# Kernel optimization log

Hardware: AMD Instinct MI355X
Metric: run time of the kernel (lower is better)

The kernel has to match this reference:

```python
import jax, jax.numpy as jnp
import numpy as np

B, S, D, H, DFF = 8, 1024, 1024, 16, 4096
DK = D // H
NEG = -1000000000.0


def layernorm(x, g, b, eps=1e-5):
    mu = jnp.mean(x, axis=-1, keepdims=True)
    var = jnp.mean((x - mu) ** 2, axis=-1, keepdims=True)
    return (x - mu) / jnp.sqrt(var + eps) * g + b


def setup_inputs() -> dict:
    key = jax.random.key(0)
    ks = jax.random.split(key, 16)
    s = 0.02
    inp = {
        "x": jax.random.normal(ks[0], (B, S, D), jnp.float32),
        "binary_mask": jax.random.randint(ks[1], (B, S), 0, 2, jnp.int32),
        # per-head projections stacked: [H, D, DK]
        "Wq": jax.random.normal(ks[2], (H, D, DK), jnp.float32) * s,
        "bq": jnp.zeros((H, DK), jnp.float32),
        "Wk": jax.random.normal(ks[3], (H, D, DK), jnp.float32) * s,
        "bk": jnp.zeros((H, DK), jnp.float32),
        "Wv": jax.random.normal(ks[4], (H, D, DK), jnp.float32) * s,
        "bv": jnp.zeros((H, DK), jnp.float32),
        "Wo": jax.random.normal(ks[5], (D, D), jnp.float32) * s,
        "bo": jnp.zeros((D,), jnp.float32),
        "ga": jnp.ones((D,), jnp.float32),
        "ba": jnp.zeros((D,), jnp.float32),
        "W1": jax.random.normal(ks[6], (D, DFF), jnp.float32) * s,
        "b1": jnp.zeros((DFF,), jnp.float32),
        "W2": jax.random.normal(ks[7], (DFF, D), jnp.float32) * s,
        "b2": jnp.zeros((D,), jnp.float32),
        "gf": jnp.ones((D,), jnp.float32),
        "bf": jnp.zeros((D,), jnp.float32),
    }
    return inp


def encoder_fwd(x, binary_mask, Wq, bq, Wk, bk, Wv, bv, Wo, bo, ga, ba, W1, b1, W2, b2, gf, bf):
    # --- multi-head self-attention (heads vectorized over h axis) ---
    q = jnp.einsum("bsd,hdk->bhsk", x, Wq) + bq[None, :, None, :]
    k = jnp.einsum("bsd,hdk->bhsk", x, Wk) + bk[None, :, None, :]
    v = jnp.einsum("bsd,hdk->bhsk", x, Wv) + bv[None, :, None, :]
    score = jnp.einsum("bhik,bhjk->bhij", q, k) / jnp.sqrt(jnp.float32(DK))
    # mask: binary_mask is over KEY positions, broadcast over query dim
    score = score + jnp.where(binary_mask[:, None, None, :] == 0, NEG, 0.0)
    # NOTE: original code softmaxes over dim=1 of [B,Sq,Sk] -> the QUERY axis
    probs = jax.nn.softmax(score, axis=2)
    ctx = jnp.einsum("bhij,bhjk->bhik", probs, v)  # [B,H,S,DK]
    ctx = jnp.transpose(ctx, (0, 2, 1, 3)).reshape(x.shape[0], x.shape[1], D)
    attn_out = ctx @ Wo + bo
    y = layernorm(x + attn_out, ga, ba)
    # --- FFN ---
    h = jax.nn.relu(y @ W1 + b1)
    ffn_out = h @ W2 + b2
    return layernorm(y + ffn_out, gf, bf)


def reference(x, binary_mask, Wq, bq, Wk, bk, Wv, bv, Wo, bo, ga, ba, W1, b1, W2, b2, gf, bf):
    return encoder_fwd(x, binary_mask, Wq, bq, Wk, bk, Wv, bv, Wo, bo, ga, ba, W1, b1, W2, b2, gf, bf)
```

## Files before the change

kernel.cpp:

```cpp
#include <hip/hip_runtime.h>
#include <hip/hip_bf16.h>

typedef __bf16 bf16;
typedef __bf16 bf16x8 __attribute__((ext_vector_type(8)));
typedef __bf16 bf16x4 __attribute__((ext_vector_type(4)));
typedef float  f32x4  __attribute__((ext_vector_type(4)));

#define NB 8
#define NS 1024
#define ND 1024
#define NH 16
#define NDK 64
#define NDFF 4096

static __device__ __forceinline__ f32x4 mfma16(bf16x8 a, bf16x8 b, f32x4 c) {
    return __builtin_amdgcn_mfma_f32_16x16x32_bf16(a, b, c, 0, 0, 0);
}

#define GLDS(g, l) __builtin_amdgcn_global_load_lds( \
    (const __attribute__((address_space(1))) void*)(g), \
    (__attribute__((address_space(3))) void*)(l), 16, 0, 0)

__global__ __launch_bounds__(256) void prep_all(
    const float* __restrict__ x, const int* __restrict__ mask,
    const float* __restrict__ Wq, const float* __restrict__ Wk, const float* __restrict__ Wv,
    const float* __restrict__ Wo, const float* __restrict__ W1, const float* __restrict__ W2,
    const float* __restrict__ bq, const float* __restrict__ bk, const float* __restrict__ bv,
    bf16* __restrict__ xb, bf16* __restrict__ wqkvT, bf16* __restrict__ WoT,
    bf16* __restrict__ W1T, bf16* __restrict__ W2T, float* __restrict__ bqkv,
    int* __restrict__ newpos, int* __restrict__ Ucnt, float* __restrict__ cvec)
{
    __shared__ __align__(16) char shraw[64 * 65 * 4];
    int bid = blockIdx.x, t = threadIdx.x;
    if (bid < 8192) {
        int idx = bid * 256 + t;
        float4 v = ((const float4*)x)[idx];
        bf16x4 o = { (bf16)v.x, (bf16)v.y, (bf16)v.z, (bf16)v.w };
        ((bf16x4*)xb)[idx] = o;
    } else if (bid < 11264) {
        float (*T)[65] = (float (*)[65])shraw;
        int tb = bid - 8192;
        const float* src; bf16* dst; int srcLd, dstLd, tR, tC; bool scale = false;
        if (tb < 768) {
            int mat = tb >> 4, ty = tb & 15;
            int h = mat & 15, type = mat >> 4;
            const float* W = (type == 0) ? Wq : (type == 1 ? Wk : Wv);
            src = W + (size_t)h * ND * NDK;
            srcLd = NDK; tR = ty * 64; tC = 0;
            dst = wqkvT + ((size_t)type * 1024 + h * 64) * ND;
            dstLd = ND;
            scale = (type == 0);
        } else if (tb < 1024) {
            int b2 = tb - 768; int ty = b2 >> 4, tx = b2 & 15;
            src = Wo; srcLd = ND; tR = ty * 64; tC = tx * 64; dst = WoT; dstLd = ND;
        } else if (tb < 2048) {
            int b2 = tb - 1024; int ty = b2 >> 6, tx = b2 & 63;
            src = W1; srcLd = NDFF; tR = ty * 64; tC = tx * 64; dst = W1T; dstLd = ND;
        } else {
            int b2 = tb - 2048; int ty = b2 >> 4, tx = b2 & 15;
            src = W2; srcLd = ND; tR = ty * 64; tC = tx * 64; dst = W2T; dstLd = NDFF;
        }
        int c0 = t & 63, r0 = t >> 6;
        #pragma unroll
        for (int rr = 0; rr < 16; rr++) {
            int row = rr * 4 + r0;
            T[row][c0] = src[(size_t)(tR + row) * srcLd + tC + c0];
        }
        __syncthreads();
        #pragma unroll
        for (int cc = 0; cc < 16; cc++) {
            int col = cc * 4 + r0;
            float v = T[c0][col];
            if (scale) v *= 0.125f;
            dst[(size_t)(tC + col) * dstLd + tR + c0] = (bf16)v;
        }
    } else if (bid < 11276) {
        int n = (bid - 11264) * 256 + t;
        if (n < 3072) {
            int type = n >> 10, hk = n & 1023;
            const float* bb = (type == 0) ? bq : (type == 1 ? bk : bv);
            float v = bb[hk];
            if (type == 0) v *= 0.125f;
            bqkv[n] = v;
        }
    } else if (bid < 11284) {
        int* sums  = (int*)shraw;
        int* scans = (int*)(shraw + 1024);
        int b = bid - 11276;
        const int* mb = mask + b * NS;
        int m[4], s = 0;
        #pragma unroll
        for (int k = 0; k < 4; k++) { m[k] = (mb[t * 4 + k] != 0) ? 1 : 0; s += m[k]; }
        sums[t] = s;
        __syncthreads();
        if (t == 0) {
            int acc = 0;
            for (int i = 0; i < 256; i++) { scans[i] = acc; acc += sums[i]; }
            scans[256] = acc;
            Ucnt[b] = acc;
        }
        __syncthreads();
        int U = scans[256];
        int p = scans[t];
        #pragma unroll
        for (int k = 0; k < 4; k++) {
            int j = t * 4 + k;
            newpos[b * NS + j] = m[k] ? p : U + (j - p);
            p += m[k];
        }
    } else {
        float4 z = {0.f, 0.f, 0.f, 0.f};
        ((float4*)cvec)[(bid - 11284) * 256 + t] = z;
    }
}

__device__ __forceinline__ void gemm_bt_core(
    const bf16* __restrict__ A, const bf16* __restrict__ BT, int K,
    int rowBase, int colBase, f32x4 (&acc)[4][4], bf16* As, bf16* Bs)
{
    const int tid = threadIdx.x;
    const int lane = tid & 63, wid = tid >> 6;
    const int wr = (wid >> 1) * 64, wc = (wid & 1) * 64;
    const int lrow = lane & 15, lq = lane >> 4;
    const int srow = wid * 32 + (lane >> 3);
    const int gblk = (lane & 7) ^ ((lane >> 3) & 7);
    const bf16* Arow = A + (size_t)(rowBase + srow) * K + gblk * 8;
    const bf16* Brow = BT + (size_t)(colBase + srow) * K + gblk * 8;
    const int co0 = ((lq) ^ (lrow & 7)) * 8;
    const int co1 = ((4 + lq) ^ (lrow & 7)) * 8;
    f32x4 zz = {0.f, 0.f, 0.f, 0.f};
    #pragma unroll
    for (int i = 0; i < 4; i++)
        #pragma unroll
        for (int j = 0; j < 4; j++) acc[i][j] = zz;
    for (int k0 = 0; k0 < K; k0 += 64) {
        __syncthreads();
        #pragma unroll
        for (int it = 0; it < 4; it++)
            GLDS(Arow + (size_t)it * 8 * K + k0, As + (wid * 32 + it * 8) * 64);
        #pragma unroll
        for (int it = 0; it < 4; it++)
            GLDS(Brow + (size_t)it * 8 * K + k0, Bs + (wid * 32 + it * 8) * 64);
        __syncthreads();
        #pragma unroll
        for (int kh = 0; kh < 2; kh++) {
            const int co = kh ? co1 : co0;
            bf16x8 af[4], bfr[4];
            #pragma unroll
            for (int tt = 0; tt < 4; tt++) {
                af[tt]  = *(const bf16x8*)&As[(wr + tt * 16 + lrow) * 64 + co];
                bfr[tt] = *(const bf16x8*)&Bs[(wc + tt * 16 + lrow) * 64 + co];
            }
            #pragma unroll
            for (int i = 0; i < 4; i++)
                #pragma unroll
                for (int j = 0; j < 4; j++)
                    acc[i][j] = mfma16(af[i], bfr[j], acc[i][j]);
        }
    }
}

__device__ __forceinline__ void gemm8p(
    const bf16* __restrict__ A, const bf16* __restrict__ BT, int K,
    int rowBase, int colBase, f32x4 (&acc)[8][4], bf16* As, bf16* Bs)
{
    constexpr int SETSZ = 256 * 64;
    const int tid = threadIdx.x, lane = tid & 63, wid = tid >> 6;
    const int wm = wid >> 2, wn = wid & 3;
    const int lrow = lane & 15, lq = lane >> 4;
    const int s8 = lane >> 3, gblk = (lane & 7) ^ s8;
    const int co0 = (lq ^ (lrow & 7)) * 8;
    const int co1 = ((4 + lq) ^ (lrow & 7)) * 8;
    f32x4 zz = {0.f, 0.f, 0.f, 0.f};
    #pragma unroll
    for (int i = 0; i < 8; i++)
        #pragma unroll
        for (int j = 0; j < 4; j++) acc[i][j] = zz;
    const bf16* Ag = A  + (size_t)(rowBase + wid * 8 + s8) * K + gblk * 8;
    const bf16* Bg = BT + (size_t)(colBase + wid * 8 + s8) * K + gblk * 8;

#define SG_A(kt, set, h) do { \
    GLDS(Ag + (size_t)((h) * 128) * K + (kt) * 64, \
         As + (set) * SETSZ + ((h) * 128 + wid * 8) * 64); \
    GLDS(Ag + (size_t)((h) * 128 + 64) * K + (kt) * 64, \
         As + (set) * SETSZ + ((h) * 128 + 64 + wid * 8) * 64); \
} while (0)
#define SG_B(kt, set, h) do { \
    GLDS(Bg + (size_t)((h) * 128) * K + (kt) * 64, \
         Bs + (set) * SETSZ + ((h) * 128 + wid * 8) * 64); \
    GLDS(Bg + (size_t)((h) * 128 + 64) * K + (kt) * 64, \
         Bs + (set) * SETSZ + ((h) * 128 + 64 + wid * 8) * 64); \
} while (0)
#define RD_A(dst, base, ms) do { _Pragma("unroll") for (int i_ = 0; i_ < 4; i_++) { \
    int ro_ = (wm * 128 + (ms) * 64 + i_ * 16 + lrow) * 64; \
    dst[i_][0] = *(const bf16x8*)&(base)[ro_ + co0]; \
    dst[i_][1] = *(const bf16x8*)&(base)[ro_ + co1]; } } while (0)
#define RD_B(dst, base, ns) do { _Pragma("unroll") for (int j_ = 0; j_ < 2; j_++) { \
    int ro_ = (wn * 64 + (ns) * 32 + j_ * 16 + lrow) * 64; \
    dst[j_][0] = *(const bf16x8*)&(base)[ro_ + co0]; \
    dst[j_][1] = *(const bf16x8*)&(base)[ro_ + co1]; } } while (0)
#define CL8(av, bv, ms, ns) do { \
    __builtin_amdgcn_s_setprio(1); \
    _Pragma("unroll") for (int i_ = 0; i_ < 4; i_++) \
    _Pragma("unroll") for (int j_ = 0; j_ < 2; j_++) { \
        acc[(ms) * 4 + i_][(ns) * 2 + j_] = \
            mfma16(av[i_][0], bv[j_][0], acc[(ms) * 4 + i_][(ns) * 2 + j_]); \
        acc[(ms) * 4 + i_][(ns) * 2 + j_] = \
            mfma16(av[i_][1], bv[j_][1], acc[(ms) * 4 + i_][(ns) * 2 + j_]); } \
    __builtin_amdgcn_s_setprio(0); \
} while (0)
#define BAR8 __builtin_amdgcn_s_barrier()
#define VM4 asm volatile("s_waitcnt vmcnt(4)" ::: "memory")
#define VM0 asm volatile("s_waitcnt vmcnt(0)" ::: "memory")

    const int nt = K >> 6, nIter = nt >> 1;
    SG_B(0, 0, 0); SG_B(0, 0, 1);
    SG_A(0, 0, 0); SG_A(0, 0, 1);
    SG_B(1, 1, 0); SG_B(1, 1, 1);
    VM4; BAR8;
    const bf16* A0b = As;           const bf16* B0b = Bs;
    const bf16* A1b = As + SETSZ;   const bf16* B1b = Bs + SETSZ;
    for (int J = 0; J < nIter; ++J) {
        const int v = 2 * J + 1;
        const bool pf = (J + 1 < nIter);
        bf16x8 a0[4][2], a1[4][2], b0[2][2], b1[2][2];
        RD_A(a0, A0b, 0); RD_B(b0, B0b, 0);
        SG_A(v, 1, 0);
        BAR8; CL8(a0, b0, 0, 0); BAR8;
        RD_B(b1, B0b, 1);
        SG_A(v, 1, 1);
        BAR8; CL8(a0, b1, 0, 1); BAR8;
        RD_A(a1, A0b, 1);
        if (pf) SG_B(v + 1, 0, 0);
        BAR8; CL8(a1, b1, 1, 1); BAR8;
        if (pf) SG_B(v + 1, 0, 1);
        BAR8; CL8(a1, b0, 1, 0);
        if (pf) { VM4; } else { VM0; }
        BAR8;
        RD_A(a0, A1b, 0); RD_B(b0, B1b, 0);
        if (pf) SG_A(v + 1, 0, 0);
        BAR8; CL8(a0, b0, 0, 0); BAR8;
        RD_B(b1, B1b, 1);
        if (pf) SG_A(v + 1, 0, 1);
        BAR8; CL8(a0, b1, 0, 1); BAR8;
        RD_A(a1, A1b, 1);
        if (pf) SG_B(v + 2, 1, 0);
        BAR8; CL8(a1, b1, 1, 1); BAR8;
        if (pf) SG_B(v + 2, 1, 1);
        BAR8; CL8(a1, b0, 1, 0);
        if (pf) { VM4; } else { VM0; }
        BAR8;
    }
#undef SG_A
#undef SG_B
#undef RD_A
#undef RD_B
#undef CL8
#undef BAR8
#undef VM4
#undef VM0
}

__device__ __forceinline__ void gemmB_core(
    const bf16* __restrict__ A, const bf16* __restrict__ BT, int K,
    int rowBase, int colBase, f32x4 (&acc)[4][4], bf16* As, bf16* Bs)
{
    constexpr int ABUF = 128 * 64, BBUF = 256 * 64;
    const int tid = threadIdx.x, lane = tid & 63, wid = tid >> 6;
    const int wm = wid >> 2, wn = wid & 3;
    const int lrow = lane & 15, lq = lane >> 4;
    const int srow = lane >> 3, gblk = (lane & 7) ^ srow;
    const int co0 = (lq ^ (lrow & 7)) * 8;
    const int co1 = ((4 + lq) ^ (lrow & 7)) * 8;
    f32x4 zz = {0.f, 0.f, 0.f, 0.f};
    #pragma unroll
    for (int i = 0; i < 4; i++)
        #pragma unroll
        for (int j = 0; j < 4; j++) acc[i][j] = zz;
    const bf16* Ag = A  + (size_t)(rowBase + wid * 8 + srow) * K + gblk * 8;
    const bf16* Bg = BT + (size_t)(colBase + wid * 8 + srow) * K + gblk * 8;

#define SGA2(kt, bi, rr) GLDS(Ag + (size_t)(kt) * 64 + (size_t)(rr) * 64 * K, \
                              As + (bi) * ABUF + ((rr) * 64 + wid * 8) * 64)
#define SGB2(kt, bi, rr) GLDS(Bg + (size_t)(kt) * 64 + (size_t)(rr) * 64 * K, \
                              Bs + (bi) * BBUF + ((rr) * 64 + wid * 8) * 64)
#define RDA2() do { _Pragma("unroll") for (int i_ = 0; i_ < 4; i_++) { \
    int ro_ = (wm * 64 + i_ * 16 + lrow) * 64; \
    af[i_][0] = *(const bf16x8*)&Ab[ro_ + co0]; \
    af[i_][1] = *(const bf16x8*)&Ab[ro_ + co1]; } } while (0)
#define RDB2(dst, NS_) do { _Pragma("unroll") for (int j_ = 0; j_ < 2; j_++) { \
    int ro_ = (wn * 64 + (NS_) * 32 + j_ * 16 + lrow) * 64; \
    dst[j_][0] = *(const bf16x8*)&Bb[ro_ + co0]; \
    dst[j_][1] = *(const bf16x8*)&Bb[ro_ + co1]; } } while (0)
#define CLUSTER_B(bfx, JO) do { \
    __builtin_amdgcn_s_barrier(); \
    asm volatile("s_waitcnt lgkmcnt(0)" ::: "memory"); \
    __builtin_amdgcn_sched_barrier(0); \
    __builtin_amdgcn_s_setprio(1); \
    _Pragma("unroll") \
    for (int i_ = 0; i_ < 4; i_++) \
        _Pragma("unroll") \
        for (int j_ = 0; j_ < 2; j_++) { \
            acc[i_][(JO) + j_] = mfma16(af[i_][0], bfx[j_][0], acc[i_][(JO) + j_]); \
            acc[i_][(JO) + j_] = mfma16(af[i_][1], bfx[j_][1], acc[i_][(JO) + j_]); \
        } \
    __builtin_amdgcn_s_setprio(0); \
} while (0)

    const int nt = K >> 6;
    SGA2(0, 0, 0); SGA2(0, 0, 1);
    SGB2(0, 0, 0); SGB2(0, 0, 1); SGB2(0, 0, 2); SGB2(0, 0, 3);
    SGA2(1, 1, 0); SGA2(1, 1, 1);
    SGB2(1, 1, 0); SGB2(1, 1, 1); SGB2(1, 1, 2); SGB2(1, 1, 3);
    asm volatile("s_waitcnt vmcnt(6)" ::: "memory");
    __builtin_amdgcn_s_barrier();

    int ci = 0, si = 2;
    for (int t = 0; t < nt; ++t) {
        const bf16* Ab = As + ci * ABUF;
        const bf16* Bb = Bs + ci * BBUF;
        const bool pf = (t + 2 < nt);
        bf16x8 af[4][2], bf0[2][2], bf1[2][2];
        RDA2(); RDB2(bf0, 0);
        if (pf) { SGA2(t + 2, si, 0); SGA2(t + 2, si, 1); SGB2(t + 2, si, 0); SGB2(t + 2, si, 1); }
        CLUSTER_B(bf0, 0);
        __builtin_amdgcn_s_barrier();
        RDB2(bf1, 1);
        if (pf) { SGB2(t + 2, si, 2); SGB2(t + 2, si, 3); }
        CLUSTER_B(bf1, 2);
        if (pf)                asm volatile("s_waitcnt vmcnt(6)" ::: "memory");
        else if (t + 1 < nt)   asm volatile("s_waitcnt vmcnt(0)" ::: "memory");
        __builtin_amdgcn_s_barrier();
        ci = (ci == 2) ? 0 : ci + 1;
        si = (si == 2) ? 0 : si + 1;
    }
#undef SGA2
#undef SGB2
#undef RDA2
#undef RDB2
#undef CLUSTER_B
}

__global__ __launch_bounds__(512, 2) void g1_qkv(
    const bf16* __restrict__ x, const bf16* __restrict__ wqkvT, const float* __restrict__ bqkv,
    const int* __restrict__ newpos,
    bf16* __restrict__ Q, bf16* __restrict__ Kb, bf16* __restrict__ Vb)
{
    __shared__ bf16 As[3 * 128 * 64], Bs[3 * 256 * 64];
    f32x4 acc[4][4];
    int g = blockIdx.x;
    int sw = (g & 7) * 96 + (g >> 3);
    int bm = sw / 12, bn = sw % 12;
    int rowBase = bm * 128, colBase = bn * 256;
    gemmB_core(x, wqkvT, ND, rowBase, colBase, acc, As, Bs);
    const int tid = threadIdx.x, lane = tid & 63, wid = tid >> 6;
    const int wm = wid >> 2, wn = wid & 3, lrow = lane & 15, lq = lane >> 4;
    const int type = colBase >> 10;
    int spv[4][4];
    if (type != 0) {
        #pragma unroll
        for (int i = 0; i < 4; i++)
            #pragma unroll
            for (int r = 0; r < 4; r++) {
                int grow = rowBase + wm * 64 + i * 16 + lq * 4 + r;
                spv[i][r] = newpos[grow];
            }
    }
    #pragma unroll
    for (int j = 0; j < 4; j++) {
        int gcol = colBase + wn * 64 + j * 16 + lrow;
        float bias = bqkv[gcol];
        int h = (gcol >> 6) & 15, kk = gcol & 63;
        bf16* dst = (type == 0) ? Q : (type == 1 ? Kb : Vb);
        #pragma unroll
        for (int i = 0; i < 4; i++) {
            #pragma unroll
            for (int r = 0; r < 4; r++) {
                int grow = rowBase + wm * 64 + i * 16 + lq * 4 + r;
                int b = grow >> 10;
                int s = (type == 0) ? (grow & 1023) : spv[i][r];
                dst[((size_t)(b * NH + h) * NS + s) * NDK + kk] = (bf16)(acc[i][j][r] + bias);
            }
        }
    }
}

__global__ __launch_bounds__(256) void vt_trans(
    const bf16* __restrict__ Vb, const int* __restrict__ Ucnt,
    bf16* __restrict__ Vt, float* __restrict__ cvec)
{
    __shared__ bf16 T[64 * 72];
    __shared__ float red[4][64];
    int bh = blockIdx.y, s0 = blockIdx.x * 64;
    const bf16* src = Vb + ((size_t)bh * NS + s0) * NDK;
    int tid = threadIdx.x;
    #pragma unroll
    for (int it = 0; it < 2; it++) {
        int g = tid + it * 256;
        int row = g >> 3, c = (g & 7) * 8;
        *(bf16x8*)&T[row * 72 + c] = *(const bf16x8*)&src[row * NDK + c];
    }
    __syncthreads();
    #pragma unroll
    for (int it = 0; it < 2; it++) {
        int g = tid + it * 256;
        int kk = g >> 3, sc = (g & 7) * 8;
        bf16x8 v;
        #pragma unroll
        for (int t = 0; t < 8; t++) v[t] = T[(sc + t) * 72 + kk];
        *(bf16x8*)&Vt[((size_t)bh * NDK + kk) * NS + s0 + sc] = v;
    }
    int U = Ucnt[bh >> 4];
    int lo = U - s0;
    if (lo < 0) lo = 0;
    if (lo < 64) {
        int kk = tid & 63, ss = tid >> 6;
        float a = 0.f;
        for (int r = lo + ss; r < 64; r += 4) a += (float)T[r * 72 + kk];
        red[ss][kk] = a;
        __syncthreads();
        if (ss == 0)
            atomicAdd(&cvec[bh * 64 + kk], red[0][kk] + red[1][kk] + red[2][kk] + red[3][kk]);
    }
}

__global__ __launch_bounds__(256) void g2_stats(
    const bf16* __restrict__ Q, const bf16* __restrict__ Kb,
    const int* __restrict__ Ucnt, float2* __restrict__ alpha)
{
    __shared__ bf16 Qs[128 * 64];
    int bh = blockIdx.y, b = bh >> 4;
    int jBase = blockIdx.x * 128;
    int U = Ucnt[b];
    const int tid = threadIdx.x;
    if (jBase >= U) {
        if (tid < 128) {
            float2 z; z.x = 0.f; z.y = 0.f;
            alpha[(size_t)bh * NS + jBase + tid] = z;
        }
        return;
    }
    const bf16* Kp = Kb + (size_t)bh * NS * NDK;
    const bf16* Qp = Q + (size_t)bh * NS * NDK;
    const int lane = tid & 63, wid = tid >> 6;
    const int lrow = lane & 15, lq = lane >> 4;
    bf16x8 kf[2][2];
    #pragma unroll
    for (int jt = 0; jt < 2; jt++)
        #pragma unroll
        for (int kh = 0; kh < 2; kh++)
            kf[jt][kh] = *(const bf16x8*)&Kp[(size_t)(jBase + wid * 32 + jt * 16 + lrow) * NDK + kh * 32 + lq * 8];
    const int srow = lane >> 3;
    const int gblk = (lane & 7) ^ srow;
    float Lacc[2][4];
    #pragma unroll
    for (int jt = 0; jt < 2; jt++)
        #pragma unroll
        for (int r = 0; r < 4; r++) Lacc[jt][r] = 0.f;
    f32x4 zz = {0.f, 0.f, 0.f, 0.f};
    for (int i0 = 0; i0 < NS; i0 += 128) {
        __syncthreads();
        #pragma unroll
        for (int it = 0; it < 4; it++)
            GLDS(Qp + (size_t)(i0 + wid * 32 + it * 8 + srow) * NDK + gblk * 8,
                 Qs + (wid * 32 + it * 8) * 64);
        __syncthreads();
        #pragma unroll
        for (int it = 0; it < 8; it++) {
            bf16x8 qb[2];
            #pragma unroll
            for (int kh = 0; kh < 2; kh++)
                qb[kh] = *(const bf16x8*)&Qs[(it * 16 + lrow) * 64 + ((kh * 4 + lq) ^ (lrow & 7)) * 8];
            #pragma unroll
            for (int jt = 0; jt < 2; jt++) {
                f32x4 s = mfma16(kf[jt][0], qb[0], zz);
                s = mfma16(kf[jt][1], qb[1], s);
                #pragma unroll
                for (int r = 0; r < 4; r++) Lacc[jt][r] += __expf(s[r]);
            }
        }
    }
    #pragma unroll
    for (int jt = 0; jt < 2; jt++) {
        #pragma unroll
        for (int r = 0; r < 4; r++) {
            float v = Lacc[jt][r];
            v += __shfl_xor(v, 1); v += __shfl_xor(v, 2);
            v += __shfl_xor(v, 4); v += __shfl_xor(v, 8);
            if (lrow == 0) {
                int j = jBase + wid * 32 + jt * 16 + lq * 4 + r;
                float2 ac;
                ac.x = (j < U) ? 1.f / v : 0.f;
                ac.y = 0.f;
                alpha[(size_t)bh * NS + j] = ac;
            }
        }
    }
}

__global__ __launch_bounds__(256) void g3_ctx(
    const bf16* __restrict__ Q, const bf16* __restrict__ Kb, const bf16* __restrict__ Vt,
    const float2* __restrict__ alpha, const int* __restrict__ Ucnt,
    const float* __restrict__ cvec, bf16* __restrict__ ctx)
{
    __shared__ bf16 Ks[64 * 64];
    __shared__ bf16 Vs[64 * 64];
    __shared__ bf16 Ps[4 * 64 * 64];
    int bh = blockIdx.y, iBase = blockIdx.x * 256;
    int b = bh >> 4, h = bh & 15;
    int U = Ucnt[b];
    int Ur = (U + 63) & ~63;
    const bf16* Qp = Q + (size_t)bh * NS * NDK;
    const bf16* Kp = Kb + (size_t)bh * NS * NDK;
    const bf16* Vp = Vt + (size_t)bh * NDK * NS;
    const float2* al = alpha + (size_t)bh * NS;
    const int tid = threadIdx.x, lane = tid & 63, wid = tid >> 6;
    const int lrow = lane & 15, lq = lane >> 4;
    const int iw = iBase + wid * 64;
    bf16x8 qf[4][2];
    #pragma unroll
    for (int it = 0; it < 4; it++)
        #pragma unroll
        for (int kh = 0; kh < 2; kh++)
            qf[it][kh] = *(const bf16x8*)&Qp[(size_t)(iw + it * 16 + lrow) * NDK + kh * 32 + lq * 8];
    const int srow = lane >> 3;
    const int gblk = (lane & 7) ^ srow;
    f32x4 cacc[4][4];
    f32x4 zz = {0.f, 0.f, 0.f, 0.f};
    #pragma unroll
    for (int it = 0; it < 4; it++)
        #pragma unroll
        for (int kt = 0; kt < 4; kt++) cacc[it][kt] = zz;
    bf16* Pw = Ps + wid * 64 * 64;
    for (int j0 = 0; j0 < Ur; j0 += 64) {
        __syncthreads();
        #pragma unroll
        for (int it = 0; it < 2; it++)
            GLDS(Kp + (size_t)(j0 + wid * 16 + it * 8 + srow) * NDK + gblk * 8,
                 Ks + (wid * 16 + it * 8) * 64);
        #pragma unroll
        for (int it = 0; it < 2; it++)
            GLDS(Vp + (size_t)(wid * 16 + it * 8 + srow) * NS + j0 + gblk * 8,
                 Vs + (wid * 16 + it * 8) * 64);
        __syncthreads();
        bf16x8 kb[4][2];
        #pragma unroll
        for (int jt = 0; jt < 4; jt++)
            #pragma unroll
            for (int kh = 0; kh < 2; kh++)
                kb[jt][kh] = *(const bf16x8*)&Ks[(jt * 16 + lrow) * 64 + ((kh * 4 + lq) ^ (lrow & 7)) * 8];
        #pragma unroll
        for (int jt = 0; jt < 4; jt++) {
            float2 acj[4];
            #pragma unroll
            for (int r = 0; r < 4; r++) acj[r] = al[j0 + jt * 16 + lq * 4 + r];
            #pragma unroll
            for (int it = 0; it < 4; it++) {
                f32x4 s = mfma16(kb[jt][0], qf[it][0], zz);
                s = mfma16(kb[jt][1], qf[it][1], s);
                bf16x4 pv;
                #pragma unroll
                for (int r = 0; r < 4; r++)
                    pv[r] = (bf16)(acj[r].x * __expf(s[r]) + acj[r].y);
                int i = it * 16 + lrow;
                int jb = jt * 2 + (lq >> 1);
                *(bf16x4*)&Pw[i * 64 + ((jb ^ (i & 7)) * 8) + (lq & 1) * 4] = pv;
            }
        }
        bf16x8 vb[4][2];
        #pragma unroll
        for (int kt = 0; kt < 4; kt++)
            #pragma unroll
            for (int kh = 0; kh < 2; kh++)
                vb[kt][kh] = *(const bf16x8*)&Vs[(kt * 16 + lrow) * 64 + ((kh * 4 + lq) ^ (lrow & 7)) * 8];
        #pragma unroll
        for (int it = 0; it < 4; it++) {
            bf16x8 pa[2];
            #pragma unroll
            for (int kh = 0; kh < 2; kh++)
                pa[kh] = *(const bf16x8*)&Pw[(it * 16 + lrow) * 64 + ((kh * 4 + lq) ^ (lrow & 7)) * 8];
            #pragma unroll
            for (int kt = 0; kt < 4; kt++) {
                cacc[it][kt] = mfma16(pa[0], vb[kt][0], cacc[it][kt]);
                cacc[it][kt] = mfma16(pa[1], vb[kt][1], cacc[it][kt]);
            }
        }
    }
    #pragma unroll
    for (int kt = 0; kt < 4; kt++) {
        int col = h * NDK + kt * 16 + lrow;
        float cv = cvec[bh * 64 + kt * 16 + lrow] * (1.f / 1024.f);
        #pragma unroll
        for (int it = 0; it < 4; it++) {
            #pragma unroll
            for (int r = 0; r < 4; r++) {
                int i = iw + it * 16 + lq * 4 + r;
                ctx[(size_t)(b * NS + i) * ND + col] = (bf16)(cacc[it][kt][r] + cv);
            }
        }
    }
}

__global__ __launch_bounds__(256) void g4_proj(
    const bf16* __restrict__ ctx, const bf16* __restrict__ WoT, const float* __restrict__ bo,
    const bf16* __restrict__ xb, bf16* __restrict__ t1b)
{
    __shared__ bf16 As[128 * 64], Bs[128 * 64];
    f32x4 acc[4][4];
    int rowBase = blockIdx.x * 128, colBase = blockIdx.y * 128;
    gemm_bt_core(ctx, WoT, ND, rowBase, colBase, acc, As, Bs);
    const int tid = threadIdx.x, lane = tid & 63, wid = tid >> 6;
    const int wr = (wid >> 1) * 64, wc = (wid & 1) * 64, lrow = lane & 15, lq = lane >> 4;
    #pragma unroll
    for (int j = 0; j < 4; j++) {
        int gcol = colBase + wc + j * 16 + lrow;
        float bias = bo[gcol];
        #pragma unroll
        for (int i = 0; i < 4; i++) {
            #pragma unroll
            for (int r = 0; r < 4; r++) {
                int grow = rowBase + wr + i * 16 + lq * 4 + r;
                float v = acc[i][j][r] + bias + (float)xb[(size_t)grow * ND + gcol];
                t1b[(size_t)grow * ND + gcol] = (bf16)v;
            }
        }
    }
}

__global__ __launch_bounds__(512, 2) void g5_ffn1(
    const bf16* __restrict__ y, const bf16* __restrict__ W1T, const float* __restrict__ b1,
    bf16* __restrict__ hb)
{
    __shared__ bf16 As[2 * 256 * 64], Bs[2 * 256 * 64];
    f32x4 acc[8][4];
    int g = blockIdx.x;
    int sw = (g & 7) * 64 + (g >> 3);
    int bm = sw >> 4, bn = sw & 15;
    int rowBase = bm * 256, colBase = bn * 256;
    gemm8p(y, W1T, ND, rowBase, colBase, acc, As, Bs);
    const int tid = threadIdx.x, lane = tid & 63, wid = tid >> 6;
    const int wm = wid >> 2, wn = wid & 3, lrow = lane & 15, lq = lane >> 4;
    #pragma unroll
    for (int j = 0; j < 4; j++) {
        int gcol = colBase + wn * 64 + j * 16 + lrow;
        float bias = b1[gcol];
        #pragma unroll
        for (int i = 0; i < 8; i++) {
            #pragma unroll
            for (int r = 0; r < 4; r++) {
                int grow = rowBase + wm * 128 + i * 16 + lq * 4 + r;
                float v = fmaxf(acc[i][j][r] + bias, 0.f);
                hb[(size_t)grow * NDFF + gcol] = (bf16)v;
            }
        }
    }
}

__global__ __launch_bounds__(512, 2) void g6_ffn2(
    const bf16* __restrict__ hb, const bf16* __restrict__ W2T, const float* __restrict__ b2,
    const bf16* __restrict__ yb, bf16* __restrict__ zb)
{
    __shared__ bf16 As[3 * 128 * 64], Bs[3 * 256 * 64];
    f32x4 acc[4][4];
    int g = blockIdx.x;
    int sw = (g & 7) * 32 + (g >> 3);
    int bm = sw >> 2, bn = sw & 3;
    int rowBase = bm * 128, colBase = bn * 256;
    gemmB_core(hb, W2T, NDFF, rowBase, colBase, acc, As, Bs);
    const int tid = threadIdx.x, lane = tid & 63, wid = tid >> 6;
    const int wm = wid >> 2, wn = wid & 3, lrow = lane & 15, lq = lane >> 4;
    #pragma unroll
    for (int j = 0; j < 4; j++) {
        int gcol = colBase + wn * 64 + j * 16 + lrow;
        float bias = b2[gcol];
        #pragma unroll
        for (int i = 0; i < 4; i++) {
            #pragma unroll
            for (int r = 0; r < 4; r++) {
                int grow = rowBase + wm * 64 + i * 16 + lq * 4 + r;
                float v = acc[i][j][r] + bias + (float)yb[(size_t)grow * ND + gcol];
                zb[(size_t)grow * ND + gcol] = (bf16)v;
            }
        }
    }
}

__global__ __launch_bounds__(256) void ln_kernel(
    const bf16* __restrict__ in, bf16* __restrict__ outb, float* __restrict__ outf,
    const float* __restrict__ g, const float* __restrict__ bb)
{
    int row = blockIdx.x, tid = threadIdx.x;
    const bf16* p = in + (size_t)row * ND;
    bf16x4 v4 = *(const bf16x4*)&p[tid * 4];
    float vv[4] = {(float)v4[0], (float)v4[1], (float)v4[2], (float)v4[3]};
    float s = vv[0] + vv[1] + vv[2] + vv[3];
    float q = vv[0]*vv[0] + vv[1]*vv[1] + vv[2]*vv[2] + vv[3]*vv[3];
    #pragma unroll
    for (int m = 1; m < 64; m <<= 1) { s += __shfl_xor(s, m); q += __shfl_xor(q, m); }
    __shared__ float rs[4], rq[4];
    int wid = tid >> 6, lane = tid & 63;
    if (lane == 0) { rs[wid] = s; rq[wid] = q; }
    __syncthreads();
    s = rs[0] + rs[1] + rs[2] + rs[3];
    q = rq[0] + rq[1] + rq[2] + rq[3];
    float mean = s * (1.f / 1024.f);
    float var = q * (1.f / 1024.f) - mean * mean;
    float rstd = 1.f / sqrtf(var + 1e-5f);
    float4 of;
    bf16x4 ob;
    #pragma unroll
    for (int k = 0; k < 4; k++) {
        int col = tid * 4 + k;
        float yv = (vv[k] - mean) * rstd * g[col] + bb[col];
        ((float*)&of)[k] = yv;
        ob[k] = (bf16)yv;
    }
    if (outb) *(bf16x4*)&outb[(size_t)row * ND + tid * 4] = ob;
    if (outf) ((float4*)(outf + (size_t)row * ND))[tid] = of;
}

extern "C" void kernel_launch(void* const* d_in, const int* in_sizes, int n_in,
                              void* d_out, int out_size, void* d_ws, size_t ws_size,
                              hipStream_t stream)
{
    const float* x    = (const float*)d_in[0];
    const int*   mask = (const int*)d_in[1];
    const float* Wq   = (const float*)d_in[2];
    const float* bq   = (const float*)d_in[3];
    const float* Wk   = (const float*)d_in[4];
    const float* bk   = (const float*)d_in[5];
    const float* Wv   = (const float*)d_in[6];
    const float* bv   = (const float*)d_in[7];
    const float* Wo   = (const float*)d_in[8];
    const float* bo   = (const float*)d_in[9];
    const float* ga   = (const float*)d_in[10];
    const float* ba   = (const float*)d_in[11];
    const float* W1   = (const float*)d_in[12];
    const float* b1   = (const float*)d_in[13];
    const float* W2   = (const float*)d_in[14];
    const float* b2   = (const float*)d_in[15];
    const float* gf   = (const float*)d_in[16];
    const float* bfb  = (const float*)d_in[17];

    size_t off = 0;
    auto alloc = [&](size_t n) { char* p = (char*)d_ws + off; off += (n + 255) & ~(size_t)255; return (void*)p; };
    bf16*   wqkvT = (bf16*)  alloc((size_t)3072 * 1024 * 2);
    bf16*   WoT   = (bf16*)  alloc((size_t)1024 * 1024 * 2);
    bf16*   W1T   = (bf16*)  alloc((size_t)4096 * 1024 * 2);
    bf16*   W2T   = (bf16*)  alloc((size_t)1024 * 4096 * 2);
    float*  bqkv  = (float*) alloc(3072 * 4);
    float2* alpha = (float2*)alloc((size_t)NB * NH * NS * 8);
    int*    newpos= (int*)   alloc((size_t)NB * NS * 4);
    int*    Ucnt  = (int*)   alloc(NB * 4);
    float*  cvec  = (float*) alloc((size_t)NB * NH * NDK * 4);
    bf16*   xb    = (bf16*)  alloc((size_t)8192 * 1024 * 2);
    bf16*   ub    = (bf16*)  alloc((size_t)8192 * 4096 * 2);
    bf16*   Qb    = ub;
    bf16*   Kb    = ub + (size_t)8192 * 1024;
    bf16*   Vt    = ub + (size_t)2 * 8192 * 1024;
    bf16*   ctx   = ub + (size_t)3 * 8192 * 1024;
    bf16*   hb    = ub;
    bf16*   t1b   = (bf16*)  alloc((size_t)8192 * 1024 * 2);
    bf16*   Vb    = t1b;
    bf16*   zb    = t1b;
    bf16*   yb    = (bf16*)  alloc((size_t)8192 * 1024 * 2);

    prep_all<<<11292, 256, 0, stream>>>(x, mask, Wq, Wk, Wv, Wo, W1, W2, bq, bk, bv,
                                        xb, wqkvT, WoT, W1T, W2T, bqkv, newpos, Ucnt, cvec);
    g1_qkv<<<768, 512, 0, stream>>>(xb, wqkvT, bqkv, newpos, Qb, Kb, Vb);
    vt_trans<<<dim3(16, 128), 256, 0, stream>>>(Vb, Ucnt, Vt, cvec);
    g2_stats<<<dim3(8, 128), 256, 0, stream>>>(Qb, Kb, Ucnt, alpha);
    g3_ctx<<<dim3(4, 128), 256, 0, stream>>>(Qb, Kb, Vt, alpha, Ucnt, cvec, ctx);
    g4_proj<<<dim3(64, 8), 256, 0, stream>>>(ctx, WoT, bo, xb, t1b);
    ln_kernel<<<8192, 256, 0, stream>>>(t1b, yb, nullptr, ga, ba);
    g5_ffn1<<<512, 512, 0, stream>>>(yb, W1T, b1, hb);
    g6_ffn2<<<256, 512, 0, stream>>>(hb, W2T, b2, yb, zb);
    ln_kernel<<<8192, 256, 0, stream>>>(zb, nullptr, (float*)d_out, gf, bfb);
}
```

Before: 472.8 us.

## Fuse layernorms into GEMM kernels via grid barrier and merge V-transpose with stats

```diff
diff --git a/kernel.cpp b/kernel.cpp
--- a/kernel.cpp
+++ b/kernel.cpp
@@ -28,7 +28,8 @@
     const float* __restrict__ bq, const float* __restrict__ bk, const float* __restrict__ bv,
     bf16* __restrict__ xb, bf16* __restrict__ wqkvT, bf16* __restrict__ WoT,
     bf16* __restrict__ W1T, bf16* __restrict__ W2T, float* __restrict__ bqkv,
-    int* __restrict__ newpos, int* __restrict__ Ucnt, float* __restrict__ cvec)
+    int* __restrict__ newpos, int* __restrict__ Ucnt, float* __restrict__ cvec,
+    int* __restrict__ ctrs)
 {
     __shared__ __align__(16) char shraw[64 * 65 * 4];
     int bid = blockIdx.x, t = threadIdx.x;
@@ -111,53 +112,88 @@
     } else {
         float4 z = {0.f, 0.f, 0.f, 0.f};
         ((float4*)cvec)[(bid - 11284) * 256 + t] = z;
-    }
-}
-
-__device__ __forceinline__ void gemm_bt_core(
+        if (bid == 11284 && t < 2) ctrs[t] = 0;
+    }
+}
+
+__device__ __forceinline__ void gemmB_core(
     const bf16* __restrict__ A, const bf16* __restrict__ BT, int K,
     int rowBase, int colBase, f32x4 (&acc)[4][4], bf16* As, bf16* Bs)
 {
-    const int tid = threadIdx.x;
-    const int lane = tid & 63, wid = tid >> 6;
-    const int wr = (wid >> 1) * 64, wc = (wid & 1) * 64;
+    constexpr int ABUF = 128 * 64, BBUF = 256 * 64;
+    const int tid = threadIdx.x, lane = tid & 63, wid = tid >> 6;
+    const int wm = wid >> 2, wn = wid & 3;
     const int lrow = lane & 15, lq = lane >> 4;
-    const int srow = wid * 32 + (lane >> 3);
-    const int gblk = (lane & 7) ^ ((lane >> 3) & 7);
-    const bf16* Arow = A + (size_t)(rowBase + srow) * K + gblk * 8;
-    const bf16* Brow = BT + (size_t)(colBase + srow) * K + gblk * 8;
-    const int co0 = ((lq) ^ (lrow & 7)) * 8;
+    const int srow = lane >> 3, gblk = (lane & 7) ^ srow;
+    const int co0 = (lq ^ (lrow & 7)) * 8;
     const int co1 = ((4 + lq) ^ (lrow & 7)) * 8;
     f32x4 zz = {0.f, 0.f, 0.f, 0.f};
     #pragma unroll
     for (int i = 0; i < 4; i++)
         #pragma unroll
         for (int j = 0; j < 4; j++) acc[i][j] = zz;
-    for (int k0 = 0; k0 < K; k0 += 64) {
-        __syncthreads();
-        #pragma unroll
-        for (int it = 0; it < 4; it++)
-            GLDS(Arow + (size_t)it * 8 * K + k0, As + (wid * 32 + it * 8) * 64);
-        #pragma unroll
-        for (int it = 0; it < 4; it++)
-            GLDS(Brow + (size_t)it * 8 * K + k0, Bs + (wid * 32 + it * 8) * 64);
-        __syncthreads();
-        #pragma unroll
-        for (int kh = 0; kh < 2; kh++) {
-            const int co = kh ? co1 : co0;
-            bf16x8 af[4], bfr[4];
-            #pragma unroll
-            for (int tt = 0; tt < 4; tt++) {
-                af[tt]  = *(const bf16x8*)&As[(wr + tt * 16 + lrow) * 64 + co];
-                bfr[tt] = *(const bf16x8*)&Bs[(wc + tt * 16 + lrow) * 64 + co];
-            }
-            #pragma unroll
-            for (int i = 0; i < 4; i++)
-                #pragma unroll
-                for (int j = 0; j < 4; j++)
-                    acc[i][j] = mfma16(af[i], bfr[j], acc[i][j]);
-        }
-    }
+    const bf16* Ag = A  + (size_t)(rowBase + wid * 8 + srow) * K + gblk * 8;
+    const bf16* Bg = BT + (size_t)(colBase + wid * 8 + srow) * K + gblk * 8;
+
+#define SGA2(kt, bi, rr) GLDS(Ag + (size_t)(kt) * 64 + (size_t)(rr) * 64 * K, \
+                              As + (bi) * ABUF + ((rr) * 64 + wid * 8) * 64)
+#define SGB2(kt, bi, rr) GLDS(Bg + (size_t)(kt) * 64 + (size_t)(rr) * 64 * K, \
+                              Bs + (bi) * BBUF + ((rr) * 64 + wid * 8) * 64)
+#define RDA2() do { _Pragma("unroll") for (int i_ = 0; i_ < 4; i_++) { \
+    int ro_ = (wm * 64 + i_ * 16 + lrow) * 64; \
+    af[i_][0] = *(const bf16x8*)&Ab[ro_ + co0]; \
+    af[i_][1] = *(const bf16x8*)&Ab[ro_ + co1]; } } while (0)
+#define RDB2(dst, NS_) do { _Pragma("unroll") for (int j_ = 0; j_ < 2; j_++) { \
+    int ro_ = (wn * 64 + (NS_) * 32 + j_ * 16 + lrow) * 64; \
+    dst[j_][0] = *(const bf16x8*)&Bb[ro_ + co0]; \
+    dst[j_][1] = *(const bf16x8*)&Bb[ro_ + co1]; } } while (0)
+#define CLUSTER_B(bfx, JO) do { \
+    __builtin_amdgcn_s_barrier(); \
+    asm volatile("s_waitcnt lgkmcnt(0)" ::: "memory"); \
+    __builtin_amdgcn_sched_barrier(0); \
+    __builtin_amdgcn_s_setprio(1); \
+    _Pragma("unroll") \
+    for (int i_ = 0; i_ < 4; i_++) \
+        _Pragma("unroll") \
+        for (int j_ = 0; j_ < 2; j_++) { \
+            acc[i_][(JO) + j_] = mfma16(af[i_][0], bfx[j_][0], acc[i_][(JO) + j_]); \
+            acc[i_][(JO) + j_] = mfma16(af[i_][1], bfx[j_][1], acc[i_][(JO) + j_]); \
+        } \
+    __builtin_amdgcn_s_setprio(0); \
+} while (0)
+
+    const int nt = K >> 6;
+    SGA2(0, 0, 0); SGA2(0, 0, 1);
+    SGB2(0, 0, 0); SGB2(0, 0, 1); SGB2(0, 0, 2); SGB2(0, 0, 3);
+    SGA2(1, 1, 0); SGA2(1, 1, 1);
+    SGB2(1, 1, 0); SGB2(1, 1, 1); SGB2(1, 1, 2); SGB2(1, 1, 3);
+    asm volatile("s_waitcnt vmcnt(6)" ::: "memory");
+    __builtin_amdgcn_s_barrier();
+
+    int ci = 0, si = 2;
+    for (int t = 0; t < nt; ++t) {
+        const bf16* Ab = As + ci * ABUF;
+        const bf16* Bb = Bs + ci * BBUF;
+        const bool pf = (t + 2 < nt);
+        bf16x8 af[4][2], bf0[2][2], bf1[2][2];
+        RDA2(); RDB2(bf0, 0);
+        if (pf) { SGA2(t + 2, si, 0); SGA2(t + 2, si, 1); SGB2(t + 2, si, 0); SGB2(t + 2, si, 1); }
+        CLUSTER_B(bf0, 0);
+        __builtin_amdgcn_s_barrier();
+        RDB2(bf1, 1);
+        if (pf) { SGB2(t + 2, si, 2); SGB2(t + 2, si, 3); }
+        CLUSTER_B(bf1, 2);
+        if (pf)                asm volatile("s_waitcnt vmcnt(6)" ::: "memory");
+        else if (t + 1 < nt)   asm volatile("s_waitcnt vmcnt(0)" ::: "memory");
+        __builtin_amdgcn_s_barrier();
+        ci = (ci == 2) ? 0 : ci + 1;
+        si = (si == 2) ? 0 : si + 1;
+    }
+#undef SGA2
+#undef SGB2
+#undef RDA2
+#undef RDB2
+#undef CLUSTER_B
 }
 
 __device__ __forceinline__ void gemm8p(
@@ -261,84 +297,61 @@
 #undef VM0
 }
 
-__device__ __forceinline__ void gemmB_core(
-    const bf16* __restrict__ A, const bf16* __restrict__ BT, int K,
-    int rowBase, int colBase, f32x4 (&acc)[4][4], bf16* As, bf16* Bs)
-{
-    constexpr int ABUF = 128 * 64, BBUF = 256 * 64;
-    const int tid = threadIdx.x, lane = tid & 63, wid = tid >> 6;
-    const int wm = wid >> 2, wn = wid & 3;
-    const int lrow = lane & 15, lq = lane >> 4;
-    const int srow = lane >> 3, gblk = (lane & 7) ^ srow;
-    const int co0 = (lq ^ (lrow & 7)) * 8;
-    const int co1 = ((4 + lq) ^ (lrow & 7)) * 8;
-    f32x4 zz = {0.f, 0.f, 0.f, 0.f};
-    #pragma unroll
-    for (int i = 0; i < 4; i++)
-        #pragma unroll
-        for (int j = 0; j < 4; j++) acc[i][j] = zz;
-    const bf16* Ag = A  + (size_t)(rowBase + wid * 8 + srow) * K + gblk * 8;
-    const bf16* Bg = BT + (size_t)(colBase + wid * 8 + srow) * K + gblk * 8;
-
-#define SGA2(kt, bi, rr) GLDS(Ag + (size_t)(kt) * 64 + (size_t)(rr) * 64 * K, \
-                              As + (bi) * ABUF + ((rr) * 64 + wid * 8) * 64)
-#define SGB2(kt, bi, rr) GLDS(Bg + (size_t)(kt) * 64 + (size_t)(rr) * 64 * K, \
-                              Bs + (bi) * BBUF + ((rr) * 64 + wid * 8) * 64)
-#define RDA2() do { _Pragma("unroll") for (int i_ = 0; i_ < 4; i_++) { \
-    int ro_ = (wm * 64 + i_ * 16 + lrow) * 64; \
-    af[i_][0] = *(const bf16x8*)&Ab[ro_ + co0]; \
-    af[i_][1] = *(const bf16x8*)&Ab[ro_ + co1]; } } while (0)
-#define RDB2(dst, NS_) do { _Pragma("unroll") for (int j_ = 0; j_ < 2; j_++) { \
-    int ro_ = (wn * 64 + (NS_) * 32 + j_ * 16 + lrow) * 64; \
-    dst[j_][0] = *(const bf16x8*)&Bb[ro_ + co0]; \
-    dst[j_][1] = *(const bf16x8*)&Bb[ro_ + co1]; } } while (0)
-#define CLUSTER_B(bfx, JO) do { \
-    __builtin_amdgcn_s_barrier(); \
-    asm volatile("s_waitcnt lgkmcnt(0)" ::: "memory"); \
-    __builtin_amdgcn_sched_barrier(0); \
-    __builtin_amdgcn_s_setprio(1); \
-    _Pragma("unroll") \
-    for (int i_ = 0; i_ < 4; i_++) \
-        _Pragma("unroll") \
-        for (int j_ = 0; j_ < 2; j_++) { \
-            acc[i_][(JO) + j_] = mfma16(af[i_][0], bfx[j_][0], acc[i_][(JO) + j_]); \
-            acc[i_][(JO) + j_] = mfma16(af[i_][1], bfx[j_][1], acc[i_][(JO) + j_]); \
-        } \
-    __builtin_amdgcn_s_setprio(0); \
-} while (0)
-
-    const int nt = K >> 6;
-    SGA2(0, 0, 0); SGA2(0, 0, 1);
-    SGB2(0, 0, 0); SGB2(0, 0, 1); SGB2(0, 0, 2); SGB2(0, 0, 3);
-    SGA2(1, 1, 0); SGA2(1, 1, 1);
-    SGB2(1, 1, 0); SGB2(1, 1, 1); SGB2(1, 1, 2); SGB2(1, 1, 3);
-    asm volatile("s_waitcnt vmcnt(6)" ::: "memory");
-    __builtin_amdgcn_s_barrier();
-
-    int ci = 0, si = 2;
-    for (int t = 0; t < nt; ++t) {
-        const bf16* Ab = As + ci * ABUF;
-        const bf16* Bb = Bs + ci * BBUF;
-        const bool pf = (t + 2 < nt);
-        bf16x8 af[4][2], bf0[2][2], bf1[2][2];
-        RDA2(); RDB2(bf0, 0);
-        if (pf) { SGA2(t + 2, si, 0); SGA2(t + 2, si, 1); SGB2(t + 2, si, 0); SGB2(t + 2, si, 1); }
-        CLUSTER_B(bf0, 0);
-        __builtin_amdgcn_s_barrier();
-        RDB2(bf1, 1);
-        if (pf) { SGB2(t + 2, si, 2); SGB2(t + 2, si, 3); }
-        CLUSTER_B(bf1, 2);
-        if (pf)                asm volatile("s_waitcnt vmcnt(6)" ::: "memory");
-        else if (t + 1 < nt)   asm volatile("s_waitcnt vmcnt(0)" ::: "memory");
-        __builtin_amdgcn_s_barrier();
-        ci = (ci == 2) ? 0 : ci + 1;
-        si = (si == 2) ? 0 : si + 1;
-    }
-#undef SGA2
-#undef SGB2
-#undef RDA2
-#undef RDB2
-#undef CLUSTER_B
+__device__ __forceinline__ void grid_rendezvous(int* ctr, int nblocks)
+{
+    __threadfence();
+    __syncthreads();
+    if (threadIdx.x == 0) {
+        atomicAdd(ctr, 1);
+        while (atomicAdd(ctr, 0) < nblocks) __builtin_amdgcn_s_sleep(8);
+    }
+    __syncthreads();
+    __threadfence();
+}
+
+template<bool WRITE_F32>
+__device__ __forceinline__ void ln_rows(
+    const bf16* __restrict__ in, bf16* __restrict__ outb, float* __restrict__ outf,
+    const float* gv, const float* bv, int rowBase)
+{
+    const int lane = threadIdx.x & 63, wid = threadIdx.x >> 6;
+    #pragma unroll
+    for (int it = 0; it < 4; it++) {
+        int row = rowBase + it * 8 + wid;
+        const bf16* p = in + (size_t)row * ND + lane * 16;
+        bf16x8 v0 = *(const bf16x8*)p;
+        bf16x8 v1 = *(const bf16x8*)(p + 8);
+        float vv[16];
+        float s = 0.f, q = 0.f;
+        #pragma unroll
+        for (int k = 0; k < 8; k++) { vv[k] = (float)v0[k]; vv[8 + k] = (float)v1[k]; }
+        #pragma unroll
+        for (int k = 0; k < 16; k++) { s += vv[k]; q += vv[k] * vv[k]; }
+        #pragma unroll
+        for (int m = 1; m < 64; m <<= 1) { s += __shfl_xor(s, m); q += __shfl_xor(q, m); }
+        float mean = s * (1.f / 1024.f);
+        float var = q * (1.f / 1024.f) - mean * mean;
+        float rstd = 1.f / sqrtf(var + 1e-5f);
+        if (WRITE_F32) {
+            float4 o[4];
+            #pragma unroll
+            for (int k = 0; k < 16; k++)
+                ((float*)o)[k] = (vv[k] - mean) * rstd * gv[k] + bv[k];
+            float* dst = outf + (size_t)row * ND + lane * 16;
+            #pragma unroll
+            for (int k = 0; k < 4; k++) ((float4*)dst)[k] = o[k];
+        } else {
+            bf16x8 o0, o1;
+            #pragma unroll
+            for (int k = 0; k < 8; k++) {
+                o0[k] = (bf16)((vv[k] - mean) * rstd * gv[k] + bv[k]);
+                o1[k] = (bf16)((vv[8 + k] - mean) * rstd * gv[8 + k] + bv[8 + k]);
+            }
+            bf16* dst = outb + (size_t)row * ND + lane * 16;
+            *(bf16x8*)dst = o0;
+            *(bf16x8*)(dst + 8) = o1;
+        }
+    }
 }
 
 __global__ __launch_bounds__(512, 2) void g1_qkv(
@@ -385,54 +398,52 @@
     }
 }
 
-__global__ __launch_bounds__(256) void vt_trans(
-    const bf16* __restrict__ Vb, const int* __restrict__ Ucnt,
+__global__ __launch_bounds__(256) void g2v(
+    const bf16* __restrict__ Q, const bf16* __restrict__ Kb, const bf16* __restrict__ Vb,
+    const int* __restrict__ Ucnt, float2* __restrict__ alpha,
     bf16* __restrict__ Vt, float* __restrict__ cvec)
 {
-    __shared__ bf16 T[64 * 72];
-    __shared__ float red[4][64];
-    int bh = blockIdx.y, s0 = blockIdx.x * 64;
-    const bf16* src = Vb + ((size_t)bh * NS + s0) * NDK;
-    int tid = threadIdx.x;
-    #pragma unroll
-    for (int it = 0; it < 2; it++) {
-        int g = tid + it * 256;
-        int row = g >> 3, c = (g & 7) * 8;
-        *(bf16x8*)&T[row * 72 + c] = *(const bf16x8*)&src[row * NDK + c];
-    }
-    __syncthreads();
-    #pragma unroll
-    for (int it = 0; it < 2; it++) {
-        int g = tid + it * 256;
-        int kk = g >> 3, sc = (g & 7) * 8;
-        bf16x8 v;
-        #pragma unroll
-        for (int t = 0; t < 8; t++) v[t] = T[(sc + t) * 72 + kk];
-        *(bf16x8*)&Vt[((size_t)bh * NDK + kk) * NS + s0 + sc] = v;
-    }
-    int U = Ucnt[bh >> 4];
-    int lo = U - s0;
-    if (lo < 0) lo = 0;
-    if (lo < 64) {
-        int kk = tid & 63, ss = tid >> 6;
-        float a = 0.f;
-        for (int r = lo + ss; r < 64; r += 4) a += (float)T[r * 72 + kk];
-        red[ss][kk] = a;
+    __shared__ __align__(16) char sraw[128 * 64 * 2];
+    int bh = blockIdx.y, b = bh >> 4;
+    const int tid = threadIdx.x;
+    if (blockIdx.x >= 8) {
+        bf16* T = (bf16*)sraw;
+        float (*red)[64] = (float (*)[64])(sraw + 64 * 72 * 2);
+        int s0 = (blockIdx.x - 8) * 64;
+        const bf16* src = Vb + ((size_t)bh * NS + s0) * NDK;
+        #pragma unroll
+        for (int it = 0; it < 2; it++) {
+            int g = tid + it * 256;
+            int row = g >> 3, c = (g & 7) * 8;
+            *(bf16x8*)&T[row * 72 + c] = *(const bf16x8*)&src[row * NDK + c];
+        }
         __syncthreads();
-        if (ss == 0)
-            atomicAdd(&cvec[bh * 64 + kk], red[0][kk] + red[1][kk] + red[2][kk] + red[3][kk]);
-    }
-}
-
-__global__ __launch_bounds__(256) void g2_stats(
-    const bf16* __restrict__ Q, const bf16* __restrict__ Kb,
-    const int* __restrict__ Ucnt, float2* __restrict__ alpha)
-{
-    __shared__ bf16 Qs[128 * 64];
-    int bh = blockIdx.y, b = bh >> 4;
+        #pragma unroll
+        for (int it = 0; it < 2; it++) {
+            int g = tid + it * 256;
+            int kk = g >> 3, sc = (g & 7) * 8;
+            bf16x8 v;
+            #pragma unroll
+            for (int t = 0; t < 8; t++) v[t] = T[(sc + t) * 72 + kk];
+            *(bf16x8*)&Vt[((size_t)bh * NDK + kk) * NS + s0 + sc] = v;
+        }
+        int U = Ucnt[b];
+        int lo = U - s0;
+        if (lo < 0) lo = 0;
+        if (lo < 64) {
+            int kk = tid & 63, ss = tid >> 6;
+            float a = 0.f;
+            for (int r = lo + ss; r < 64; r += 4) a += (float)T[r * 72 + kk];
+            red[ss][kk] = a;
+            __syncthreads();
+            if (ss == 0)
+                atomicAdd(&cvec[bh * 64 + kk], red[0][kk] + red[1][kk] + red[2][kk] + red[3][kk]);
+        }
+        return;
+    }
+    bf16* Qs = (bf16*)sraw;
     int jBase = blockIdx.x * 128;
     int U = Ucnt[b];
-    const int tid = threadIdx.x;
     if (jBase >= U) {
         if (tid < 128) {
             float2 z; z.x = 0.f; z.y = 0.f;
@@ -601,30 +612,43 @@
     }
 }
 
-__global__ __launch_bounds__(256) void g4_proj(
+__global__ __launch_bounds__(512, 2) void g4_proj(
     const bf16* __restrict__ ctx, const bf16* __restrict__ WoT, const float* __restrict__ bo,
-    const bf16* __restrict__ xb, bf16* __restrict__ t1b)
-{
-    __shared__ bf16 As[128 * 64], Bs[128 * 64];
+    const bf16* __restrict__ xb, bf16* __restrict__ t1b,
+    const float* __restrict__ ga, const float* __restrict__ ba,
+    bf16* __restrict__ yb, int* __restrict__ ctr)
+{
+    __shared__ bf16 As[3 * 128 * 64], Bs[3 * 256 * 64];
     f32x4 acc[4][4];
-    int rowBase = blockIdx.x * 128, colBase = blockIdx.y * 128;
-    gemm_bt_core(ctx, WoT, ND, rowBase, colBase, acc, As, Bs);
+    int g = blockIdx.x;
+    int sw = (g & 7) * 32 + (g >> 3);
+    int bm = sw >> 2, bn = sw & 3;
+    int rowBase = bm * 128, colBase = bn * 256;
+    gemmB_core(ctx, WoT, ND, rowBase, colBase, acc, As, Bs);
     const int tid = threadIdx.x, lane = tid & 63, wid = tid >> 6;
-    const int wr = (wid >> 1) * 64, wc = (wid & 1) * 64, lrow = lane & 15, lq = lane >> 4;
+    const int wm = wid >> 2, wn = wid & 3, lrow = lane & 15, lq = lane >> 4;
     #pragma unroll
     for (int j = 0; j < 4; j++) {
-        int gcol = colBase + wc + j * 16 + lrow;
+        int gcol = colBase + wn * 64 + j * 16 + lrow;
         float bias = bo[gcol];
         #pragma unroll
         for (int i = 0; i < 4; i++) {
             #pragma unroll
             for (int r = 0; r < 4; r++) {
-                int grow = rowBase + wr + i * 16 + lq * 4 + r;
+                int grow = rowBase + wm * 64 + i * 16 + lq * 4 + r;
                 float v = acc[i][j][r] + bias + (float)xb[(size_t)grow * ND + gcol];
                 t1b[(size_t)grow * ND + gcol] = (bf16)v;
             }
         }
     }
+    float gv[16], bv[16];
+    #pragma unroll
+    for (int k = 0; k < 16; k++) {
+        int col = lane * 16 + k;
+        gv[k] = ga[col]; bv[k] = ba[col];
+    }
+    grid_rendezvous(ctr, 256);
+    ln_rows<false>(t1b, yb, nullptr, gv, bv, blockIdx.x * 32);
 }
 
 __global__ __launch_bounds__(512, 2) void g5_ffn1(
@@ -658,7 +682,9 @@
 
 __global__ __launch_bounds__(512, 2) void g6_ffn2(
     const bf16* __restrict__ hb, const bf16* __restrict__ W2T, const float* __restrict__ b2,
-    const bf16* __restrict__ yb, bf16* __restrict__ zb)
+    const bf16* __restrict__ yb, bf16* __restrict__ zb,
+    const float* __restrict__ gf, const float* __restrict__ bfb,
+    float* __restrict__ outf, int* __restrict__ ctr)
 {
     __shared__ bf16 As[3 * 128 * 64], Bs[3 * 256 * 64];
     f32x4 acc[4][4];
@@ -683,40 +709,14 @@
             }
         }
     }
-}
-
-__global__ __launch_bounds__(256) void ln_kernel(
-    const bf16* __restrict__ in, bf16* __restrict__ outb, float* __restrict__ outf,
-    const float* __restrict__ g, const float* __restrict__ bb)
-{
-    int row = blockIdx.x, tid = threadIdx.x;
-    const bf16* p = in + (size_t)row * ND;
-    bf16x4 v4 = *(const bf16x4*)&p[tid * 4];
-    float vv[4] = {(float)v4[0], (float)v4[1], (float)v4[2], (float)v4[3]};
-    float s = vv[0] + vv[1] + vv[2] + vv[3];
-    float q = vv[0]*vv[0] + vv[1]*vv[1] + vv[2]*vv[2] + vv[3]*vv[3];
-    #pragma unroll
-    for (int m = 1; m < 64; m <<= 1) { s += __shfl_xor(s, m); q += __shfl_xor(q, m); }
-    __shared__ float rs[4], rq[4];
-    int wid = tid >> 6, lane = tid & 63;
-    if (lane == 0) { rs[wid] = s; rq[wid] = q; }
-    __syncthreads();
-    s = rs[0] + rs[1] + rs[2] + rs[3];
-    q = rq[0] + rq[1] + rq[2] + rq[3];
-    float mean = s * (1.f / 1024.f);
-    float var = q * (1.f / 1024.f) - mean * mean;
-    float rstd = 1.f / sqrtf(var + 1e-5f);
-    float4 of;
-    bf16x4 ob;
-    #pragma unroll
-    for (int k = 0; k < 4; k++) {
-        int col = tid * 4 + k;
-        float yv = (vv[k] - mean) * rstd * g[col] + bb[col];
-        ((float*)&of)[k] = yv;
-        ob[k] = (bf16)yv;
-    }
-    if (outb) *(bf16x4*)&outb[(size_t)row * ND + tid * 4] = ob;
-    if (outf) ((float4*)(outf + (size_t)row * ND))[tid] = of;
+    float gv[16], bv[16];
+    #pragma unroll
+    for (int k = 0; k < 16; k++) {
+        int col = lane * 16 + k;
+        gv[k] = gf[col]; bv[k] = bfb[col];
+    }
+    grid_rendezvous(ctr, 256);
+    ln_rows<true>(zb, nullptr, outf, gv, bv, blockIdx.x * 32);
 }
 
 extern "C" void kernel_launch(void* const* d_in, const int* in_sizes, int n_in,
@@ -753,6 +753,7 @@
     int*    newpos= (int*)   alloc((size_t)NB * NS * 4);
     int*    Ucnt  = (int*)   alloc(NB * 4);
     float*  cvec  = (float*) alloc((size_t)NB * NH * NDK * 4);
+    int*    ctrs  = (int*)   alloc(8);
     bf16*   xb    = (bf16*)  alloc((size_t)8192 * 1024 * 2);
     bf16*   ub    = (bf16*)  alloc((size_t)8192 * 4096 * 2);
     bf16*   Qb    = ub;
@@ -766,14 +767,11 @@
     bf16*   yb    = (bf16*)  alloc((size_t)8192 * 1024 * 2);
 
     prep_all<<<11292, 256, 0, stream>>>(x, mask, Wq, Wk, Wv, Wo, W1, W2, bq, bk, bv,
-                                        xb, wqkvT, WoT, W1T, W2T, bqkv, newpos, Ucnt, cvec);
+                                        xb, wqkvT, WoT, W1T, W2T, bqkv, newpos, Ucnt, cvec, ctrs);
     g1_qkv<<<768, 512, 0, stream>>>(xb, wqkvT, bqkv, newpos, Qb, Kb, Vb);
-    vt_trans<<<dim3(16, 128), 256, 0, stream>>>(Vb, Ucnt, Vt, cvec);
-    g2_stats<<<dim3(8, 128), 256, 0, stream>>>(Qb, Kb, Ucnt, alpha);
+    g2v<<<dim3(24, 128), 256, 0, stream>>>(Qb, Kb, Vb, Ucnt, alpha, Vt, cvec);
     g3_ctx<<<dim3(4, 128), 256, 0, stream>>>(Qb, Kb, Vt, alpha, Ucnt, cvec, ctx);
-    g4_proj<<<dim3(64, 8), 256, 0, stream>>>(ctx, WoT, bo, xb, t1b);
-    ln_kernel<<<8192, 256, 0, stream>>>(t1b, yb, nullptr, ga, ba);
+    g4_proj<<<256, 512, 0, stream>>>(ctx, WoT, bo, xb, t1b, ga, ba, yb, ctrs);
     g5_ffn1<<<512, 512, 0, stream>>>(yb, W1T, b1, hb);
-    g6_ffn2<<<256, 512, 0, stream>>>(hb, W2T, b2, yb, zb);
-    ln_kernel<<<8192, 256, 0, stream>>>(zb, nullptr, (float*)d_out, gf, bfb);
-}
+    g6_ffn2<<<256, 512, 0, stream>>>(hb, W2T, b2, yb, zb, gf, bfb, (float*)d_out, ctrs + 1);
+}
```

After: 692.3 us. 46.4% more time.
